# Optimization experiments

Hardware: AMD Instinct MI355X
Metric: run time of the kernel (lower is better)

Reference implementation:

```python
import jax, jax.numpy as jnp
import numpy as np
import math

B, S, D, H, WIN = 2, 4096, 512, 8, 50
DK = D // H


def setup_inputs() -> dict:
    key = jax.random.key(0)
    ks = jax.random.split(key, 10)
    scale = 0.02
    return {
        "x": jax.random.normal(ks[0], (B, S, D), dtype=jnp.float32),
        "opcode_types": jax.random.randint(ks[1], (B, S), 0, 10, dtype=jnp.int64),
        "Wq": jax.random.normal(ks[2], (D, D), dtype=jnp.float32) * scale,
        "bq": jnp.zeros((D,), dtype=jnp.float32),
        "Wk": jax.random.normal(ks[3], (D, D), dtype=jnp.float32) * scale,
        "bk": jnp.zeros((D,), dtype=jnp.float32),
        "Wv": jax.random.normal(ks[4], (D, D), dtype=jnp.float32) * scale,
        "bv": jnp.zeros((D,), dtype=jnp.float32),
        "Wo": jax.random.normal(ks[5], (D, D), dtype=jnp.float32) * scale,
        "bo": jnp.zeros((D,), dtype=jnp.float32),
    }


def reference(x, opcode_types, Wq, bq, Wk, bk, Wv, bv, Wo, bo):
    b, s, d = x.shape
    # Linear projections (torch Linear: x @ W.T + b), split heads -> [B,H,S,DK]
    q = (x @ Wq.T + bq).reshape(b, s, H, DK).transpose(0, 2, 1, 3)
    k = (x @ Wk.T + bk).reshape(b, s, H, DK).transpose(0, 2, 1, 3)
    v = (x @ Wv.T + bv).reshape(b, s, H, DK).transpose(0, 2, 1, 3)

    pos = jnp.arange(s)
    window = jnp.abs(pos[:, None] - pos[None, :]) <= WIN          # [S,S]
    ctrl_cols = (opcode_types == 0).any(axis=0)                   # [S]
    allow = window | ctrl_cols[None, :]                           # [S,S]

    scores = jnp.einsum("bhqd,bhkd->bhqk", q, k) / math.sqrt(DK)  # [B,H,S,S]
    scores = jnp.where(allow[None, None], scores, jnp.float32(-1e9))
    attn = jax.nn.softmax(scores, axis=-1)
    attn = jnp.nan_to_num(attn, nan=0.0)
    out = jnp.einsum("bhqk,bhkd->bhqd", attn, v)                  # [B,H,S,DK]
    out = out.transpose(0, 2, 1, 3).reshape(b, s, d)
    return out @ Wo.T + bo
```

## Files before the change

kernel.cpp:

```cpp
#include <hip/hip_runtime.h>
#include <hip/hip_bf16.h>
#include <math.h>

#define B_ 2
#define S_ 4096
#define D_ 512
#define H_ 8
#define DK_ 64
#define WIN_ 50
#define NGT 32
#define QSCALE 0.18033688011112042f

typedef __attribute__((ext_vector_type(8))) short short8;
typedef __attribute__((ext_vector_type(4))) float f32x4;
typedef __attribute__((ext_vector_type(4))) unsigned short us4;
typedef unsigned short ushort_t;

__device__ __forceinline__ unsigned short f2bf(float f) {
    unsigned u = __builtin_bit_cast(unsigned, f);
    u += 0x7FFF + ((u >> 16) & 1);
    return (unsigned short)(u >> 16);
}
__device__ __forceinline__ float bf2f(unsigned short h) {
    return __builtin_bit_cast(float, ((unsigned)h) << 16);
}
__device__ __forceinline__ unsigned cvt_pk_bf16(float lo, float hi) {
    unsigned r;
    asm("v_cvt_pk_bf16_f32 %0, %1, %2" : "=v"(r) : "v"(lo), "v"(hi));
    return r;
}

__global__ __launch_bounds__(256) void prep_all(const float* __restrict__ x,
                                                const float* __restrict__ W0,
                                                const float* __restrict__ W1,
                                                const float* __restrict__ W2,
                                                const float* __restrict__ W3,
                                                const int* __restrict__ opcode,
                                                ushort_t* __restrict__ xh,
                                                ushort_t* __restrict__ whb,
                                                ushort_t* __restrict__ wol,
                                                int* __restrict__ glist,
                                                int* __restrict__ gcount) {
    const int bid = blockIdx.x;
    const int t = threadIdx.x;
    if (bid < 4096) {
        int i = bid * 256 + t;
        f32x4 v = ((const f32x4*)x)[i];
        us4 hv;
        for (int e = 0; e < 4; ++e) hv[e] = f2bf(v[e]);
        ((us4*)xh)[i] = hv;
    } else if (bid < 5120) {
        int b2 = bid - 4096;
        int wz = b2 >> 8, inner = b2 & 255;
        const float* src = (wz == 0) ? W0 : (wz == 1) ? W1 : (wz == 2) ? W2 : W3;
        int i = inner * 256 + t;
        f32x4 v = ((const f32x4*)src)[i];
        us4 hv, lv;
        for (int e = 0; e < 4; ++e) {
            unsigned short hb = f2bf(v[e]);
            hv[e] = hb;
            lv[e] = f2bf(v[e] - bf2f(hb));
        }
        ((us4*)(whb + (size_t)wz * D_ * D_))[i] = hv;
        if (wz == 3) ((us4*)wol)[i] = lv;
    } else {
        __shared__ int cnts[256];
        unsigned fl = 0; int c = 0;
        for (int k = 0; k < 16; ++k) {
            int col = t * 16 + k;
            int flag = (opcode[col] == 0) | (opcode[S_ + col] == 0);
            fl |= (unsigned)flag << k; c += flag;
        }
        cnts[t] = c;
        __syncthreads();
        for (int off = 1; off < 256; off <<= 1) {
            int v = cnts[t];
            int a = (t >= off) ? cnts[t - off] : 0;
            __syncthreads();
            cnts[t] = v + a;
            __syncthreads();
        }
        int base = cnts[t] - c;
        for (int k = 0; k < 16; ++k)
            if ((fl >> k) & 1) glist[base++] = t * 16 + k;
        if (t == 255) gcount[0] = cnts[255];
    }
}

__device__ __forceinline__ void gemm_core1(const ushort_t* __restrict__ A,
                                           const ushort_t* __restrict__ Bw,
                                           ushort_t (&LDS)[2][8192],
                                           int m0, int n0, int t,
                                           f32x4 (&acc)[4][4]) {
    const int lane = t & 63, wave = t >> 6;
    const int lrow = lane & 15, lkg = lane >> 4;
    const int wr = wave >> 1, wc = wave & 1;
    const ushort_t* srcs[2] = {A, Bw};
    const int row0[2] = {m0, n0};

    auto stage = [&](int buf, int k0) {
        #pragma unroll
        for (int it = 0; it < 4; ++it) {
            int c = it * 4 + wave;
            int tile = c >> 3;
            int kg = (c >> 1) & 3;
            int r = ((c & 1) << 6) | lane;
            const ushort_t* g = srcs[tile] + (size_t)(row0[tile] + r) * 512 + k0 + kg * 8;
            __builtin_amdgcn_global_load_lds(
                (const __attribute__((address_space(1))) void*)g,
                (__attribute__((address_space(3))) void*)(&LDS[buf][c * 512]),
                16, 0, 0);
        }
    };

    stage(0, 0);
    __syncthreads();

    const int aoff = lkg * 1024 + (wr * 64 + lrow) * 8;
    const int boff = 4096 + lkg * 1024 + (wc * 64 + lrow) * 8;
    int cur = 0;
    for (int ks = 0; ks < 16; ++ks) {
        if (ks < 15) stage(cur ^ 1, (ks + 1) * 32);
        const ushort_t* Lb = LDS[cur];
        short8 ah[4], bh[4];
        #pragma unroll
        for (int m = 0; m < 4; ++m) ah[m] = *(const short8*)(Lb + aoff + m * 128);
        #pragma unroll
        for (int n = 0; n < 4; ++n) bh[n] = *(const short8*)(Lb + boff + n * 128);
        #pragma unroll
        for (int m = 0; m < 4; ++m)
            #pragma unroll
            for (int n = 0; n < 4; ++n)
                acc[m][n] = __builtin_amdgcn_mfma_f32_16x16x32_bf16(ah[m], bh[n], acc[m][n], 0, 0, 0);
        __syncthreads();
        cur ^= 1;
    }
}

__device__ __forceinline__ void gemm_core3(const ushort_t* __restrict__ Ah,
                                           const ushort_t* __restrict__ Al,
                                           const ushort_t* __restrict__ Bh,
                                           const ushort_t* __restrict__ Bl,
                                           ushort_t (&LDS)[2][16384],
                                           int m0, int n0, int t,
                                           f32x4 (&acc)[4][4]) {
    const int lane = t & 63, wave = t >> 6;
    const int lrow = lane & 15, lkg = lane >> 4;
    const int wr = wave >> 1, wc = wave & 1;
    const ushort_t* srcs[4] = {Ah, Al, Bh, Bl};
    const int row0[4] = {m0, m0, n0, n0};

    auto stage = [&](int buf, int k0) {
        #pragma unroll
        for (int it = 0; it < 8; ++it) {
            int c = it * 4 + wave;
            int tile = c >> 3;
            int kg = (c >> 1) & 3;
            int r = ((c & 1) << 6) | lane;
            const ushort_t* g = srcs[tile] + (size_t)(row0[tile] + r) * 512 + k0 + kg * 8;
            __builtin_amdgcn_global_load_lds(
                (const __attribute__((address_space(1))) void*)g,
                (__attribute__((address_space(3))) void*)(&LDS[buf][c * 512]),
                16, 0, 0);
        }
    };

    stage(0, 0);
    __syncthreads();

    const int aoff = lkg * 1024 + (wr * 64 + lrow) * 8;
    const int boff = 2 * 4096 + lkg * 1024 + (wc * 64 + lrow) * 8;
    int cur = 0;
    for (int ks = 0; ks < 16; ++ks) {
        if (ks < 15) stage(cur ^ 1, (ks + 1) * 32);
        const ushort_t* Lb = LDS[cur];
        short8 ah[4], al[4], bh[4], bl[4];
        #pragma unroll
        for (int m = 0; m < 4; ++m) {
            ah[m] = *(const short8*)(Lb + aoff + m * 128);
            al[m] = *(const short8*)(Lb + 4096 + aoff + m * 128);
        }
        #pragma unroll
        for (int n = 0; n < 4; ++n) {
            bh[n] = *(const short8*)(Lb + boff + n * 128);
            bl[n] = *(const short8*)(Lb + 4096 + boff + n * 128);
        }
        #pragma unroll
        for (int m = 0; m < 4; ++m)
            #pragma unroll
            for (int n = 0; n < 4; ++n) {
                acc[m][n] = __builtin_amdgcn_mfma_f32_16x16x32_bf16(ah[m], bh[n], acc[m][n], 0, 0, 0);
                acc[m][n] = __builtin_amdgcn_mfma_f32_16x16x32_bf16(al[m], bh[n], acc[m][n], 0, 0, 0);
                acc[m][n] = __builtin_amdgcn_mfma_f32_16x16x32_bf16(ah[m], bl[n], acc[m][n], 0, 0, 0);
            }
        __syncthreads();
        cur ^= 1;
    }
}

__global__ __launch_bounds__(256) void gemm_qkv(const ushort_t* __restrict__ xh,
                                                const ushort_t* __restrict__ whb,
                                                const float* __restrict__ bq,
                                                const float* __restrict__ bk,
                                                const float* __restrict__ bv,
                                                ushort_t* __restrict__ qb,
                                                char* __restrict__ bandimg) {
    __shared__ ushort_t LDS[2][8192];
    const int z = blockIdx.z;
    const int t = threadIdx.x;
    const ushort_t* Wz = whb + (size_t)z * D_ * D_;
    const int lane = t & 63, wave = t >> 6;
    const int lrow = lane & 15, lkg = lane >> 4;
    const int wr = wave >> 1, wc = wave & 1;

    f32x4 acc[4][4];
    for (int m = 0; m < 4; ++m)
        for (int n = 0; n < 4; ++n)
            acc[m][n] = f32x4{0.f, 0.f, 0.f, 0.f};

    if (z == 2) {
        const int m0 = blockIdx.y * 128, n0 = blockIdx.x * 128;
        gemm_core1(xh, Wz, LDS, m0, n0, t, acc);
        for (int m = 0; m < 4; ++m) {
            int s_base = m0 + wr * 64 + m * 16 + lkg * 4;
            int bb = s_base >> 12, s0 = s_base & (S_ - 1);
            int jt = s0 >> 6, jr0 = s0 & 63;
            for (int n = 0; n < 4; ++n) {
                int col = n0 + wc * 64 + n * 16 + lrow;
                float bs = bv[col];
                int hh = col >> 6, dk = col & 63;
                us4 pk;
                for (int r = 0; r < 4; ++r) pk[r] = f2bf(acc[m][n][r] + bs);
                char* img = bandimg + (((size_t)(bb * H_ + hh)) * 64 + jt) * 16384 + 8192;
                *(us4*)(img + ((dk * 128 + jr0 * 2) ^ ((dk & 7) << 4))) = pk;
            }
        }
    } else {
        const int m0 = blockIdx.x * 128, n0 = blockIdx.y * 128;
        gemm_core1(Wz, xh, LDS, m0, n0, t, acc);
        const float* bias = (z == 0) ? bq : bk;
        for (int m = 0; m < 4; ++m) {
            int d_base = m0 + wr * 64 + m * 16 + lkg * 4;
            f32x4 b4 = *(const f32x4*)(bias + d_base);
            int hh = d_base >> 6, dkb = d_base & 63;
            for (int n = 0; n < 4; ++n) {
                int s = n0 + wc * 64 + n * 16 + lrow;
                int bb = s >> 12, sl = s & (S_ - 1);
                us4 pk;
                if (z == 0) {
                    for (int r = 0; r < 4; ++r) pk[r] = f2bf((acc[m][n][r] + b4[r]) * QSCALE);
                    *(us4*)(qb + (((size_t)(bb * H_ + hh) * S_) + sl) * DK_ + dkb) = pk;
                } else {
                    for (int r = 0; r < 4; ++r) pk[r] = f2bf(acc[m][n][r] + b4[r]);
                    int jt = sl >> 6, jr = sl & 63;
                    char* img = bandimg + (((size_t)(bb * H_ + hh)) * 64 + jt) * 16384;
                    *(us4*)(img + ((jr * 128 + dkb * 2) ^ ((jr & 7) << 4))) = pk;
                }
            }
        }
    }
}

__global__ __launch_bounds__(256) void gemm_fin(const ushort_t* __restrict__ Woh,
                                                const ushort_t* __restrict__ Wol,
                                                const ushort_t* __restrict__ aoh,
                                                const ushort_t* __restrict__ aol,
                                                const float* __restrict__ bias,
                                                float* __restrict__ outp) {
    __shared__ ushort_t LDS[2][16384];
    const int t = threadIdx.x;
    const int lane = t & 63, wave = t >> 6;
    const int lrow = lane & 15, lkg = lane >> 4;
    const int wr = wave >> 1, wc = wave & 1;
    const int m0 = blockIdx.x * 128, n0 = blockIdx.y * 128;

    f32x4 acc[4][4];
    for (int m = 0; m < 4; ++m)
        for (int n = 0; n < 4; ++n)
            acc[m][n] = f32x4{0.f, 0.f, 0.f, 0.f};
    gemm_core3(Woh, Wol, aoh, aol, LDS, m0, n0, t, acc);

    for (int m = 0; m < 4; ++m) {
        int d_base = m0 + wr * 64 + m * 16 + lkg * 4;
        f32x4 b4 = *(const f32x4*)(bias + d_base);
        for (int n = 0; n < 4; ++n) {
            int s = n0 + wc * 64 + n * 16 + lrow;
            f32x4 o;
            for (int r = 0; r < 4; ++r) o[r] = acc[m][n][r] + b4[r];
            *(f32x4*)(outp + (size_t)s * D_ + d_base) = o;
        }
    }
}

__global__ __launch_bounds__(256) void prep_glob(const char* __restrict__ bandimg,
                                                 char* __restrict__ globimg,
                                                 const int* __restrict__ glist,
                                                 const int* __restrict__ gcount) {
    int G = gcount[0];
    int gc = blockIdx.x;
    if (gc * 64 >= G) return;
    int h = blockIdx.y, b = blockIdx.z;
    int t = threadIdx.x;
    __shared__ int jl[64];
    if (t < 64) { int gi = gc * 64 + t; jl[t] = (gi < G) ? glist[gi] : -1; }
    __syncthreads();
    const size_t bh = (size_t)(b * H_ + h);
    char* dst = globimg + (bh * NGT + gc) * 16384;
    {
        int c = t >> 2, q = t & 3;
        int jj = jl[c];
        #pragma unroll
        for (int p = 0; p < 2; ++p) {
            int o_dst = c * 128 + q * 32 + p * 16;
            short8 val;
            if (jj >= 0) {
                int jr = jj & 63, jt = jj >> 6;
                const char* src = bandimg + (bh * 64 + jt) * 16384;
                val = *(const short8*)(src + ((jr * 128 + q * 32 + p * 16) ^ ((jr & 7) << 4)));
            } else {
                for (int e = 0; e < 8; ++e) val[e] = 0;
            }
            *(short8*)(dst + (o_dst ^ ((c & 7) << 4))) = val;
        }
    }
    {
        int d = t >> 2, qq = t & 3;
        short8 v0, v1;
        #pragma unroll 16
        for (int i = 0; i < 16; ++i) {
            int c = qq * 16 + i;
            int jj = jl[c];
            ushort_t val = 0;
            if (jj >= 0) {
                int jr = jj & 63, jt = jj >> 6;
                const char* src = bandimg + (bh * 64 + jt) * 16384 + 8192;
                val = *(const ushort_t*)(src + ((d * 128 + jr * 2) ^ ((d & 7) << 4)));
            }
            if (i < 8) v0[i] = val; else v1[i - 8] = val;
        }
        int o = d * 128 + qq * 32;
        *(short8*)(dst + 8192 + (o ^ ((d & 7) << 4))) = v0;
        *(short8*)(dst + 8192 + ((o + 16) ^ ((d & 7) << 4))) = v1;
    }
}

__global__ __launch_bounds__(512) void attn_mfma4(const ushort_t* __restrict__ Qp,
                                                  const char* __restrict__ bandimg,
                                                  const char* __restrict__ globimg,
                                                  const int* __restrict__ glist,
                                                  const int* __restrict__ gcount,
                                                  ushort_t* __restrict__ AOh,
                                                  ushort_t* __restrict__ AOl) {
    __shared__ char buf[2][16384];
    __shared__ int jl[2][64];
    __shared__ ushort_t Ps[8 * 16 * 64];

    const int t = threadIdx.x, lane = t & 63, wave = t >> 6;
    const int q = lane & 15, g = lane >> 4;
    const int i0 = blockIdx.x * 128, h = blockIdx.y, b = blockIdx.z;
    const size_t headoff = ((size_t)(b * H_ + h)) * S_ * DK_;
    const int iq = i0 + wave * 16 + q;
    const int iqm = iq - WIN_;

    short8 qa[2];
    {
        const ushort_t* qrow = Qp + headoff + (size_t)iq * DK_;
        qa[0] = *(const short8*)(qrow + 8 * g);
        qa[1] = *(const short8*)(qrow + 32 + 8 * g);
    }

    f32x4 Oa[4];
    for (int n = 0; n < 4; ++n) Oa[n] = f32x4{0.f, 0.f, 0.f, 0.f};
    float m_st = -1e30f, l_st = 0.f;

    int jlo = i0 - WIN_;
    int jt_lo = (jlo < 0) ? 0 : (jlo >> 6);
    int jhi = i0 + 127 + WIN_; if (jhi > S_ - 1) jhi = S_ - 1;
    int jt_hi = jhi >> 6;
    int nband = jt_hi - jt_lo + 1;
    const int G = gcount[0];
    int nglob = (G + 63) >> 6; if (nglob > NGT) nglob = NGT;
    int nchunk = nband + nglob;

    const size_t bh = (size_t)(b * H_ + h);

    int koff[4][2], poffw[4], poffr[2];
    #pragma unroll
    for (int n = 0; n < 4; ++n) {
        int row = n * 16 + q;
        #pragma unroll
        for (int kt = 0; kt < 2; ++kt)
            koff[n][kt] = (row * 128 + g * 16 + kt * 64) ^ ((row & 7) << 4);
        poffw[n] = (q * 128 + n * 32 + g * 8) ^ ((q & 7) << 4);
    }
    #pragma unroll
    for (int kt = 0; kt < 2; ++kt)
        poffr[kt] = (q * 128 + g * 16 + kt * 64) ^ ((q & 7) << 4);

    auto stage = [&](int ch, int nb) {
        const char* img = (ch < nband)
            ? bandimg + (bh * 64 + (jt_lo + ch)) * 16384
            : globimg + (bh * NGT + (ch - nband)) * 16384;
        #pragma unroll
        for (int i = 0; i < 2; ++i) {
            int seg = wave * 2 + i;
            __builtin_amdgcn_global_load_lds(
                (const __attribute__((address_space(1))) void*)(img + seg * 1024 + lane * 16),
                (__attribute__((address_space(3))) void*)(buf[nb] + seg * 1024),
                16, 0, 0);
        }
        if (ch >= nband && t < 64) {
            int gi = (ch - nband) * 64 + t;
            jl[nb][t] = (gi < G) ? glist[gi] : -1;
        }
    };

    stage(0, 0);
    __syncthreads();

    int cur = 0;
    for (int ch = 0; ch < nchunk; ++ch) {
        if (ch + 1 < nchunk) stage(ch + 1, cur ^ 1);
        const bool isband = ch < nband;
        const int cbase = isband ? (jt_lo + ch) * 64 : 0;
        const char* Kb = buf[cur];
        const char* Vb = buf[cur] + 8192;

        f32x4 sc[4];
        for (int n = 0; n < 4; ++n) sc[n] = f32x4{0.f, 0.f, 0.f, 0.f};
        #pragma unroll
        for (int n = 0; n < 4; ++n)
            #pragma unroll
            for (int kt = 0; kt < 2; ++kt) {
                short8 ka = *(const short8*)(Kb + koff[n][kt]);
                sc[n] = __builtin_amdgcn_mfma_f32_16x16x32_bf16(ka, qa[kt], sc[n], 0, 0, 0);
            }

        float pm = -1e30f;
        if (isband) {
            #pragma unroll
            for (int n = 0; n < 4; ++n) {
                int jb = cbase + n * 16 + 4 * g;
                #pragma unroll
                for (int r = 0; r < 4; ++r) {
                    bool inwin = (unsigned)(jb + r - iqm) <= 2 * WIN_;
                    float s = inwin ? sc[n][r] : -1e30f;
                    sc[n][r] = s;
                    pm = fmaxf(pm, s);
                }
            }
        } else {
            #pragma unroll
            for (int n = 0; n < 4; ++n) {
                int4 J = *(const int4*)(&jl[cur][n * 16 + g * 4]);
                int js[4] = {J.x, J.y, J.z, J.w};
                #pragma unroll
                for (int r = 0; r < 4; ++r) {
                    int jj = js[r];
                    bool inwin = (unsigned)(jj - iqm) <= 2 * WIN_;
                    bool allow = (jj >= 0) && !inwin;
                    float s = allow ? sc[n][r] : -1e30f;
                    sc[n][r] = s;
                    pm = fmaxf(pm, s);
                }
            }
        }
        pm = fmaxf(pm, __shfl_xor(pm, 16, 64));
        pm = fmaxf(pm, __shfl_xor(pm, 32, 64));

        bool skip = __all(pm <= m_st);
        float fac = 1.0f;
        if (!skip) {
            float mn = fmaxf(m_st, pm);
            fac = exp2f(m_st - mn);
            m_st = mn;
        }
        float rs = 0.f;
        #pragma unroll
        for (int n = 0; n < 4; ++n)
            #pragma unroll
            for (int r = 0; r < 4; ++r) {
                float p = exp2f(sc[n][r] - m_st);
                sc[n][r] = p;
                rs += p;
            }
        rs += __shfl_xor(rs, 16, 64);
        rs += __shfl_xor(rs, 32, 64);
        l_st = skip ? (l_st + rs) : (l_st * fac + rs);

        ushort_t* Pw = Ps + wave * 1024;
        #pragma unroll
        for (int n = 0; n < 4; ++n) {
            unsigned pk0 = cvt_pk_bf16(sc[n][0], sc[n][1]);
            unsigned pk1 = cvt_pk_bf16(sc[n][2], sc[n][3]);
            *(unsigned long long*)((char*)Pw + poffw[n]) =
                ((unsigned long long)pk1 << 32) | pk0;
        }

        if (!skip) {
            #pragma unroll
            for (int n = 0; n < 4; ++n)
                #pragma unroll
                for (int r = 0; r < 4; ++r) Oa[n][r] *= fac;
        }

        short8 pa[2];
        #pragma unroll
        for (int kt = 0; kt < 2; ++kt)
            pa[kt] = *(const short8*)((char*)Pw + poffr[kt]);
        #pragma unroll
        for (int n = 0; n < 4; ++n)
            #pragma unroll
            for (int kt = 0; kt < 2; ++kt) {
                short8 va = *(const short8*)(Vb + koff[n][kt]);
                Oa[n] = __builtin_amdgcn_mfma_f32_16x16x32_bf16(va, pa[kt], Oa[n], 0, 0, 0);
            }
        __syncthreads();
        cur ^= 1;
    }

    float inv = 1.0f / l_st;
    #pragma unroll
    for (int n = 0; n < 4; ++n) {
        us4 ph, pl;
        #pragma unroll
        for (int r = 0; r < 4; ++r) {
            float v = Oa[n][r] * inv;
            unsigned short hb = f2bf(v);
            ph[r] = hb;
            pl[r] = f2bf(v - bf2f(hb));
        }
        size_t base = ((size_t)b * S_ + iq) * D_ + h * DK_ + (n * 16 + g * 4);
        *(us4*)(AOh + base) = ph;
        *(us4*)(AOl + base) = pl;
    }
}

extern "C" void kernel_launch(void* const* d_in, const int* in_sizes, int n_in,
                              void* d_out, int out_size, void* d_ws, size_t ws_size,
                              hipStream_t stream) {
    const float* x      = (const float*)d_in[0];
    const int*   opcode = (const int*)d_in[1];
    const float* Wq = (const float*)d_in[2];
    const float* bq = (const float*)d_in[3];
    const float* Wk = (const float*)d_in[4];
    const float* bk = (const float*)d_in[5];
    const float* Wv = (const float*)d_in[6];
    const float* bv = (const float*)d_in[7];
    const float* Wo = (const float*)d_in[8];
    const float* bo = (const float*)d_in[9];
    float* out = (float*)d_out;

    char* ws = (char*)d_ws;
    const size_t bsd = (size_t)B_ * S_ * D_;
    const size_t bf_bytes = bsd * sizeof(ushort_t);
    const size_t w_bytes  = (size_t)D_ * D_ * sizeof(ushort_t);

    ushort_t* qb  = (ushort_t*)(ws);
    ushort_t* xh  = (ushort_t*)(ws + bf_bytes);
    ushort_t* aol = (ushort_t*)(ws + 2 * bf_bytes);
    ushort_t* aoh = xh;
    char* wbase = ws + 3 * bf_bytes;
    ushort_t* whb = (ushort_t*)wbase;
    ushort_t* wol = (ushort_t*)(wbase + 4 * w_bytes);
    char* bandimg = wbase + 5 * w_bytes;
    char* globimg = bandimg + (size_t)16 * 64 * 16384;
    int* glist  = (int*)(globimg + (size_t)16 * NGT * 16384);
    int* gcount = glist + S_;

    prep_all<<<5121, 256, 0, stream>>>(x, Wq, Wk, Wv, Wo, opcode,
                                       xh, whb, wol, glist, gcount);

    gemm_qkv<<<dim3(D_ / 128, (B_ * S_) / 128, 3), 256, 0, stream>>>(
        xh, whb, bq, bk, bv, qb, bandimg);

    prep_glob<<<dim3(NGT, H_, B_), 256, 0, stream>>>(bandimg, globimg, glist, gcount);

    attn_mfma4<<<dim3(S_ / 128, H_, B_), 512, 0, stream>>>(
        qb, bandimg, globimg, glist, gcount, aoh, aol);

    gemm_fin<<<dim3(D_ / 128, (B_ * S_) / 128), 256, 0, stream>>>(
        whb + 3 * (size_t)D_ * D_, wol, aoh, aol, bo, out);
}
```

Baseline: 204.7 us.

## Skip masking for global chunks outside window and use raw exp2

Pads the global column list with -1 and precomputes, per block, a bitmask of global chunks whose column range overlaps the block's sliding window or that are partially filled. Only those chunks get the per-element mask; the rest just take a plain max. Global indices are now read straight from global memory instead of being staged in LDS each chunk. Also replaces exp2f with a raw v_exp_f32 inline asm, and flattens the grid so blocks of the same query tile across heads are adjacent.

```diff
diff --git a/kernel.cpp b/kernel.cpp
--- a/kernel.cpp
+++ b/kernel.cpp
@@ -27,6 +27,11 @@
 __device__ __forceinline__ unsigned cvt_pk_bf16(float lo, float hi) {
     unsigned r;
     asm("v_cvt_pk_bf16_f32 %0, %1, %2" : "=v"(r) : "v"(lo), "v"(hi));
+    return r;
+}
+__device__ __forceinline__ float v_exp2(float x) {
+    float r;
+    asm("v_exp_f32 %0, %1\n\ts_nop 0" : "=v"(r) : "v"(x));
     return r;
 }
 
@@ -83,7 +88,12 @@
         int base = cnts[t] - c;
         for (int k = 0; k < 16; ++k)
             if ((fl >> k) & 1) glist[base++] = t * 16 + k;
-        if (t == 255) gcount[0] = cnts[255];
+        int G = cnts[255];
+        if (t == 255) gcount[0] = G;
+        for (int k = 0; k < 8; ++k) {
+            int idx = G + t + k * 256;
+            if (idx < S_) glist[idx] = -1;
+        }
     }
 }
 
@@ -344,7 +354,7 @@
     }
 }
 
-__global__ __launch_bounds__(512) void attn_mfma4(const ushort_t* __restrict__ Qp,
+__global__ __launch_bounds__(512) void attn_mfma5(const ushort_t* __restrict__ Qp,
                                                   const char* __restrict__ bandimg,
                                                   const char* __restrict__ globimg,
                                                   const int* __restrict__ glist,
@@ -352,12 +362,14 @@
                                                   ushort_t* __restrict__ AOh,
                                                   ushort_t* __restrict__ AOl) {
     __shared__ char buf[2][16384];
-    __shared__ int jl[2][64];
     __shared__ ushort_t Ps[8 * 16 * 64];
 
     const int t = threadIdx.x, lane = t & 63, wave = t >> 6;
     const int q = lane & 15, g = lane >> 4;
-    const int i0 = blockIdx.x * 128, h = blockIdx.y, b = blockIdx.z;
+    const int bid = blockIdx.x;
+    const int bh_lin = bid & 15;
+    const int b = bh_lin >> 3, h = bh_lin & 7;
+    const int i0 = (bid >> 4) * 128;
     const size_t headoff = ((size_t)(b * H_ + h)) * S_ * DK_;
     const int iq = i0 + wave * 16 + q;
     const int iqm = iq - WIN_;
@@ -384,6 +396,18 @@
 
     const size_t bh = (size_t)(b * H_ + h);
 
+    unsigned needmask = 0;
+    {
+        int wmin = i0 - WIN_, wmax = i0 + 127 + WIN_;
+        for (int gc = 0; gc < nglob; ++gc) {
+            int lo = glist[gc * 64];
+            int hidx = (gc * 64 + 63 < G) ? (gc * 64 + 63) : (G - 1);
+            int hi = glist[hidx];
+            bool nm = (lo <= wmax && hi >= wmin) || (gc == nglob - 1 && (G & 63));
+            needmask |= (unsigned)nm << gc;
+        }
+    }
+
     int koff[4][2], poffw[4], poffr[2];
     #pragma unroll
     for (int n = 0; n < 4; ++n) {
@@ -397,10 +421,12 @@
     for (int kt = 0; kt < 2; ++kt)
         poffr[kt] = (q * 128 + g * 16 + kt * 64) ^ ((q & 7) << 4);
 
+    const char* band_base = bandimg + (bh * 64 + jt_lo) * 16384;
+    const char* glob_base = globimg + (bh * NGT) * 16384;
+
     auto stage = [&](int ch, int nb) {
-        const char* img = (ch < nband)
-            ? bandimg + (bh * 64 + (jt_lo + ch)) * 16384
-            : globimg + (bh * NGT + (ch - nband)) * 16384;
+        const char* img = (ch < nband) ? (band_base + (size_t)ch * 16384)
+                                       : (glob_base + (size_t)(ch - nband) * 16384);
         #pragma unroll
         for (int i = 0; i < 2; ++i) {
             int seg = wave * 2 + i;
@@ -409,10 +435,6 @@
                 (__attribute__((address_space(3))) void*)(buf[nb] + seg * 1024),
                 16, 0, 0);
         }
-        if (ch >= nband && t < 64) {
-            int gi = (ch - nband) * 64 + t;
-            jl[nb][t] = (gi < G) ? glist[gi] : -1;
-        }
     };
 
     stage(0, 0);
@@ -423,6 +445,7 @@
         if (ch + 1 < nchunk) stage(ch + 1, cur ^ 1);
         const bool isband = ch < nband;
         const int cbase = isband ? (jt_lo + ch) * 64 : 0;
+        const int gbase = (ch - nband) * 64;
         const char* Kb = buf[cur];
         const char* Vb = buf[cur] + 8192;
 
@@ -436,34 +459,44 @@
                 sc[n] = __builtin_amdgcn_mfma_f32_16x16x32_bf16(ka, qa[kt], sc[n], 0, 0, 0);
             }
 
-        float pm = -1e30f;
-        if (isband) {
-            #pragma unroll
-            for (int n = 0; n < 4; ++n) {
-                int jb = cbase + n * 16 + 4 * g;
+        float pm;
+        bool nm = isband || ((needmask >> (ch - nband)) & 1);
+        if (nm) {
+            pm = -1e30f;
+            if (isband) {
                 #pragma unroll
-                for (int r = 0; r < 4; ++r) {
-                    bool inwin = (unsigned)(jb + r - iqm) <= 2 * WIN_;
-                    float s = inwin ? sc[n][r] : -1e30f;
-                    sc[n][r] = s;
-                    pm = fmaxf(pm, s);
+                for (int n = 0; n < 4; ++n) {
+                    int jb = cbase + n * 16 + 4 * g;
+                    #pragma unroll
+                    for (int r = 0; r < 4; ++r) {
+                        bool inwin = (unsigned)(jb + r - iqm) <= 2 * WIN_;
+                        float s = inwin ? sc[n][r] : -1e30f;
+                        sc[n][r] = s;
+                        pm = fmaxf(pm, s);
+                    }
                 }
+            } else {
+                #pragma unroll
+                for (int n = 0; n < 4; ++n) {
+                    int4 J = *(const int4*)(glist + gbase + n * 16 + g * 4);
+                    int js[4] = {J.x, J.y, J.z, J.w};
+                    #pragma unroll
+                    for (int r = 0; r < 4; ++r) {
+                        int jj = js[r];
+                        bool inwin = (unsigned)(jj - iqm) <= 2 * WIN_;
+                        bool allow = (jj >= 0) && !inwin;
+                        float s = allow ? sc[n][r] : -1e30f;
+                        sc[n][r] = s;
+                        pm = fmaxf(pm, s);
+                    }
+                }
             }
         } else {
-            #pragma unroll
-            for (int n = 0; n < 4; ++n) {
-                int4 J = *(const int4*)(&jl[cur][n * 16 + g * 4]);
-                int js[4] = {J.x, J.y, J.z, J.w};
-                #pragma unroll
-                for (int r = 0; r < 4; ++r) {
-                    int jj = js[r];
-                    bool inwin = (unsigned)(jj - iqm) <= 2 * WIN_;
-                    bool allow = (jj >= 0) && !inwin;
-                    float s = allow ? sc[n][r] : -1e30f;
-                    sc[n][r] = s;
-                    pm = fmaxf(pm, s);
-                }
-            }
+            float a0 = fmaxf(fmaxf(sc[0][0], sc[0][1]), fmaxf(sc[0][2], sc[0][3]));
+            float a1 = fmaxf(fmaxf(sc[1][0], sc[1][1]), fmaxf(sc[1][2], sc[1][3]));
+            float a2 = fmaxf(fmaxf(sc[2][0], sc[2][1]), fmaxf(sc[2][2], sc[2][3]));
+            float a3 = fmaxf(fmaxf(sc[3][0], sc[3][1]), fmaxf(sc[3][2], sc[3][3]));
+            pm = fmaxf(fmaxf(a0, a1), fmaxf(a2, a3));
         }
         pm = fmaxf(pm, __shfl_xor(pm, 16, 64));
         pm = fmaxf(pm, __shfl_xor(pm, 32, 64));
@@ -472,7 +505,7 @@
         float fac = 1.0f;
         if (!skip) {
             float mn = fmaxf(m_st, pm);
-            fac = exp2f(m_st - mn);
+            fac = v_exp2(m_st - mn);
             m_st = mn;
         }
         float rs = 0.f;
@@ -480,7 +513,7 @@
         for (int n = 0; n < 4; ++n)
             #pragma unroll
             for (int r = 0; r < 4; ++r) {
-                float p = exp2f(sc[n][r] - m_st);
+                float p = v_exp2(sc[n][r] - m_st);
                 sc[n][r] = p;
                 rs += p;
             }
@@ -576,7 +609,7 @@
 
     prep_glob<<<dim3(NGT, H_, B_), 256, 0, stream>>>(bandimg, globimg, glist, gcount);
 
-    attn_mfma4<<<dim3(S_ / 128, H_, B_), 512, 0, stream>>>(
+    attn_mfma5<<<dim3(512), 512, 0, stream>>>(
         qb, bandimg, globimg, glist, gcount, aoh, aol);
 
     gemm_fin<<<dim3(D_ / 128, (B_ * S_) / 128), 256, 0, stream>>>(
```

Result: faster. 196.0 us (-4.2%).
